# Kernel tuning notes

Measured on AMD Instinct MI355X. Metric: run time of the kernel, lower is better.

## Reference

```python
import jax, jax.numpy as jnp
import numpy as np

NUM_CLASSES = 3
# anchors in pixels: (w, h, im, re)
ANCHORS = np.array([[11.0, 14.0, 0.0, 1.0],
                    [24.0, 17.0, 0.0, 1.0],
                    [42.0, 27.0, 0.0, 1.0]], dtype=np.float32)
NUM_ANCHORS = ANCHORS.shape[0]
BATCH = 64
GRID = 152


def setup_inputs() -> dict:
    key = jax.random.key(0)
    ch = NUM_ANCHORS * (7 + NUM_CLASSES)  # 30
    x = jax.random.normal(key, (BATCH, ch, GRID, GRID), dtype=jnp.float32)
    return {"x": x, "img_size": 608}


def reference(x, img_size):
    # Inference path of YoloLayer.forward (targets=None): anchor decode.
    B, _, _, G = x.shape
    A, C = NUM_ANCHORS, NUM_CLASSES
    stride = img_size / G  # 608 / 152 = 4.0

    # [B, A, 7+C, G, G] -> [B, A, G, G, 7+C]
    pred = jnp.transpose(x.reshape(B, A, 7 + C, G, G), (0, 1, 3, 4, 2))

    pred_x = jax.nn.sigmoid(pred[..., 0])
    pred_y = jax.nn.sigmoid(pred[..., 1])
    pred_w = pred[..., 2]
    pred_h = pred[..., 3]
    pred_im = pred[..., 4]
    pred_re = pred[..., 5]
    pred_conf = jax.nn.sigmoid(pred[..., 6])
    pred_cls = jax.nn.sigmoid(pred[..., 7:])

    # grid offsets: grid_x varies along last (width) axis, grid_y along rows
    g = jnp.arange(G, dtype=x.dtype)
    grid_x = g[None, None, None, :]  # [1,1,1,G]
    grid_y = g[None, None, :, None]  # [1,1,G,1]

    anchors = jnp.asarray(ANCHORS, dtype=x.dtype) / stride  # scaled anchors
    anchor_w = anchors[:, 0].reshape(1, A, 1, 1)
    anchor_h = anchors[:, 1].reshape(1, A, 1, 1)

    sg = jax.lax.stop_gradient  # original uses .clone().detach() for out_boxes
    bx = sg(pred_x) + grid_x
    by = sg(pred_y) + grid_y
    bw = jnp.exp(sg(pred_w)) * anchor_w
    bh = jnp.exp(sg(pred_h)) * anchor_h
    bim = sg(pred_im)
    bre = sg(pred_re)

    n = A * G * G
    xywh = jnp.stack([bx, by, bw, bh], axis=-1).reshape(B, n, 4) * stride
    imre = jnp.stack([bim, bre], axis=-1).reshape(B, n, 2)
    conf = pred_conf.reshape(B, n, 1)
    cls_ = pred_cls.reshape(B, n, C)

    output = jnp.concatenate([xywh, imre, conf, cls_], axis=-1)  # [B, A*G*G, 6+1+C]
    return output
```

## Files before the change

kernel.cpp:

```cpp
#include <hip/hip_runtime.h>


#define NA 3
#define NC 3
#define GSZ 152
#define GG (GSZ * GSZ)
#define CH 10
#define BATCH 64
#define BLOCK 256
#define FLOATS_PER_BLOCK (BLOCK * CH)
#define VEC4_PER_BLOCK (FLOATS_PER_BLOCK / 4)

__global__ __launch_bounds__(BLOCK) void yolo_decode_kernel(
    const float* __restrict__ x,
    const int* __restrict__ img_size_p,
    float* __restrict__ out)
{
    __shared__ float lds[BLOCK * (CH + 1)];

    const int tid = threadIdx.x;
    const long long cell_g = (long long)blockIdx.x * BLOCK + tid;

    const int plane = (int)(cell_g / GG);
    const int cell  = (int)(cell_g - (long long)plane * GG);
    const int a  = plane % NA;
    const int gy = cell / GSZ;
    const int gx = cell - gy * GSZ;

    const int   iv = img_size_p[0];
    const float fv = __int_as_float(iv);
    const float img = (iv > 0 && iv < 100000) ? (float)iv : fv;
    const float stride = img / (float)GSZ;

    const float aw[NA] = {11.0f, 24.0f, 42.0f};
    const float ah[NA] = {14.0f, 17.0f, 27.0f};

    const long long base = (long long)plane * (CH * GG) + cell;
    float v[CH];
    #pragma unroll
    for (int c = 0; c < CH; ++c)
        v[c] = x[base + (long long)c * GG];

    float o[CH];
    o[0] = (1.0f / (1.0f + __expf(-v[0])) + (float)gx) * stride;
    o[1] = (1.0f / (1.0f + __expf(-v[1])) + (float)gy) * stride;
    o[2] = (__expf(v[2]) * (aw[a] / stride)) * stride;
    o[3] = (__expf(v[3]) * (ah[a] / stride)) * stride;
    o[4] = v[4];
    o[5] = v[5];
    o[6] = 1.0f / (1.0f + __expf(-v[6]));
    o[7] = 1.0f / (1.0f + __expf(-v[7]));
    o[8] = 1.0f / (1.0f + __expf(-v[8]));
    o[9] = 1.0f / (1.0f + __expf(-v[9]));

    #pragma unroll
    for (int k = 0; k < CH; ++k)
        lds[tid * (CH + 1) + k] = o[k];
    __syncthreads();

    float4* outv = (float4*)(out + (long long)blockIdx.x * FLOATS_PER_BLOCK);
    #pragma unroll
    for (int m = 0; m < 3; ++m) {
        int idx = m * BLOCK + tid;
        if (idx < VEC4_PER_BLOCK) {
            int j = idx * 4;
            float4 w;
            w.x = lds[((j    ) / CH) * (CH + 1) + ((j    ) % CH)];
            w.y = lds[((j + 1) / CH) * (CH + 1) + ((j + 1) % CH)];
            w.z = lds[((j + 2) / CH) * (CH + 1) + ((j + 2) % CH)];
            w.w = lds[((j + 3) / CH) * (CH + 1) + ((j + 3) % CH)];
            outv[idx] = w;
        }
    }
}

extern "C" void kernel_launch(void* const* d_in, const int* in_sizes, int n_in,
                              void* d_out, int out_size, void* d_ws, size_t ws_size,
                              hipStream_t stream)
{
    const float* x = (const float*)d_in[0];
    const int* img_size = (const int*)d_in[1];
    float* out = (float*)d_out;

    const long long total_cells = (long long)BATCH * NA * GG;
    const int grid = (int)(total_cells / BLOCK);

    yolo_decode_kernel<<<grid, BLOCK, 0, stream>>>(x, img_size, out);
}
```

Before: 296.1 us.

## Process four cells per thread with vectorized nontemporal loads and stores

Each thread now handles four consecutive grid cells, loading each channel as a 16-byte vector with nontemporal hints instead of scalar loads. The LDS staging layout changes to channel-major with a padded row stride, and the transposed output is written with nontemporal 16-byte stores. Block size drops to 128 threads. The aim is fewer, wider memory transactions and less cache pollution in a purely bandwidth-bound decode. In exchange each thread uses more registers, and correctness depends on GG being a multiple of 4 so the four cells never cross a plane or row boundary; 152 divisible by 4 guarantees this.

```diff
diff --git a/kernel.cpp b/kernel.cpp
--- a/kernel.cpp
+++ b/kernel.cpp
@@ -7,70 +7,80 @@
 #define GG (GSZ * GSZ)
 #define CH 10
 #define BATCH 64
-#define BLOCK 256
-#define FLOATS_PER_BLOCK (BLOCK * CH)
-#define VEC4_PER_BLOCK (FLOATS_PER_BLOCK / 4)
+#define BLOCK 128
+#define CPT 4
+#define NCELL (BLOCK * CPT)
+#define LDS_S 516
+#define LDSF (CH * LDS_S)
+
+typedef float f32x4 __attribute__((ext_vector_type(4)));
 
 __global__ __launch_bounds__(BLOCK) void yolo_decode_kernel(
     const float* __restrict__ x,
     const int* __restrict__ img_size_p,
     float* __restrict__ out)
 {
-    __shared__ float lds[BLOCK * (CH + 1)];
+    __shared__ float lds[LDSF];
 
     const int tid = threadIdx.x;
-    const long long cell_g = (long long)blockIdx.x * BLOCK + tid;
+    const int cell_g0 = blockIdx.x * NCELL + tid * CPT;
 
-    const int plane = (int)(cell_g / GG);
-    const int cell  = (int)(cell_g - (long long)plane * GG);
-    const int a  = plane % NA;
-    const int gy = cell / GSZ;
-    const int gx = cell - gy * GSZ;
+    const int plane = cell_g0 / GG;
+    const int cell0 = cell_g0 - plane * GG;
+    const int a   = plane % NA;
+    const int gy  = cell0 / GSZ;
+    const int gx0 = cell0 - gy * GSZ;
 
     const int   iv = img_size_p[0];
     const float fv = __int_as_float(iv);
     const float img = (iv > 0 && iv < 100000) ? (float)iv : fv;
     const float stride = img / (float)GSZ;
 
-    const float aw[NA] = {11.0f, 24.0f, 42.0f};
-    const float ah[NA] = {14.0f, 17.0f, 27.0f};
+    const float awa = (a == 0) ? 11.0f : (a == 1) ? 24.0f : 42.0f;
+    const float aha = (a == 0) ? 14.0f : (a == 1) ? 17.0f : 27.0f;
 
-    const long long base = (long long)plane * (CH * GG) + cell;
-    float v[CH];
+    const int base = plane * (CH * GG) + cell0;
+    f32x4 v4[CH];
     #pragma unroll
     for (int c = 0; c < CH; ++c)
-        v[c] = x[base + (long long)c * GG];
+        v4[c] = __builtin_nontemporal_load(
+            (const f32x4*)(x + base + c * GG));
+    float* v = (float*)v4;
 
-    float o[CH];
-    o[0] = (1.0f / (1.0f + __expf(-v[0])) + (float)gx) * stride;
-    o[1] = (1.0f / (1.0f + __expf(-v[1])) + (float)gy) * stride;
-    o[2] = (__expf(v[2]) * (aw[a] / stride)) * stride;
-    o[3] = (__expf(v[3]) * (ah[a] / stride)) * stride;
-    o[4] = v[4];
-    o[5] = v[5];
-    o[6] = 1.0f / (1.0f + __expf(-v[6]));
-    o[7] = 1.0f / (1.0f + __expf(-v[7]));
-    o[8] = 1.0f / (1.0f + __expf(-v[8]));
-    o[9] = 1.0f / (1.0f + __expf(-v[9]));
+    f32x4 o4[CH];
+    float* o = (float*)o4;
+    const float gyf = (float)gy;
+    #pragma unroll
+    for (int i = 0; i < CPT; ++i) {
+        const float gxf = (float)(gx0 + i);
+        o[0*4+i] = (1.0f / (1.0f + __expf(-v[0*4+i])) + gxf) * stride;
+        o[1*4+i] = (1.0f / (1.0f + __expf(-v[1*4+i])) + gyf) * stride;
+        o[2*4+i] = (__expf(v[2*4+i]) * (awa / stride)) * stride;
+        o[3*4+i] = (__expf(v[3*4+i]) * (aha / stride)) * stride;
+        o[4*4+i] = v[4*4+i];
+        o[5*4+i] = v[5*4+i];
+        o[6*4+i] = 1.0f / (1.0f + __expf(-v[6*4+i]));
+        o[7*4+i] = 1.0f / (1.0f + __expf(-v[7*4+i]));
+        o[8*4+i] = 1.0f / (1.0f + __expf(-v[8*4+i]));
+        o[9*4+i] = 1.0f / (1.0f + __expf(-v[9*4+i]));
+    }
 
     #pragma unroll
-    for (int k = 0; k < CH; ++k)
-        lds[tid * (CH + 1) + k] = o[k];
+    for (int c = 0; c < CH; ++c)
+        *(f32x4*)&lds[c * LDS_S + tid * CPT] = o4[c];
     __syncthreads();
 
-    float4* outv = (float4*)(out + (long long)blockIdx.x * FLOATS_PER_BLOCK);
+    f32x4* outv = (f32x4*)(out + (long long)blockIdx.x * (NCELL * CH));
     #pragma unroll
-    for (int m = 0; m < 3; ++m) {
-        int idx = m * BLOCK + tid;
-        if (idx < VEC4_PER_BLOCK) {
-            int j = idx * 4;
-            float4 w;
-            w.x = lds[((j    ) / CH) * (CH + 1) + ((j    ) % CH)];
-            w.y = lds[((j + 1) / CH) * (CH + 1) + ((j + 1) % CH)];
-            w.z = lds[((j + 2) / CH) * (CH + 1) + ((j + 2) % CH)];
-            w.w = lds[((j + 3) / CH) * (CH + 1) + ((j + 3) % CH)];
-            outv[idx] = w;
-        }
+    for (int it = 0; it < CH; ++it) {
+        const int idx = it * BLOCK + tid;
+        const int j = idx * 4;
+        f32x4 w;
+        w.x = lds[((j    ) % CH) * LDS_S + ((j    ) / CH)];
+        w.y = lds[((j + 1) % CH) * LDS_S + ((j + 1) / CH)];
+        w.z = lds[((j + 2) % CH) * LDS_S + ((j + 2) / CH)];
+        w.w = lds[((j + 3) % CH) * LDS_S + ((j + 3) / CH)];
+        __builtin_nontemporal_store(w, outv + idx);
     }
 }
 
@@ -83,7 +93,7 @@
     float* out = (float*)d_out;
 
     const long long total_cells = (long long)BATCH * NA * GG;
-    const int grid = (int)(total_cells / BLOCK);
+    const int grid = (int)(total_cells / NCELL);
 
     yolo_decode_kernel<<<grid, BLOCK, 0, stream>>>(x, img_size, out);
 }
```

Result: faster. 283.0 us (-4.4%).
